# Kernel tuning notes

Measured on AMD Instinct MI355X. Metric: run time of the kernel, lower is better.

Reference implementation:

```python
import jax, jax.numpy as jnp
import numpy as np

EMBED_DIM = 1024
NUM_HEADS = 16
HEAD_DIM = EMBED_DIM // NUM_HEADS
QUANTUM_HEADS = 2
BATCH = 2
SEQ = 2048


def setup_inputs() -> dict:
    key = jax.random.key(0)
    ks = jax.random.split(key, 12)
    s = 1.0 / np.sqrt(EMBED_DIM)
    d = {
        "x": jax.random.normal(ks[0], (BATCH, SEQ, EMBED_DIM), jnp.float32),
        "Wq": jax.random.normal(ks[1], (EMBED_DIM, EMBED_DIM), jnp.float32) * s,
        "bq": jax.random.normal(ks[2], (EMBED_DIM,), jnp.float32) * s,
        "Wk": jax.random.normal(ks[3], (EMBED_DIM, EMBED_DIM), jnp.float32) * s,
        "bk": jax.random.normal(ks[4], (EMBED_DIM,), jnp.float32) * s,
        "Wv": jax.random.normal(ks[5], (EMBED_DIM, EMBED_DIM), jnp.float32) * s,
        "bv": jax.random.normal(ks[6], (EMBED_DIM,), jnp.float32) * s,
        "Wo": jax.random.normal(ks[7], (EMBED_DIM, EMBED_DIM), jnp.float32) * s,
        "bo": jax.random.normal(ks[8], (EMBED_DIM,), jnp.float32) * s,
        # surrogate params for the per-head quantum expectation layers
        "qw": jax.random.normal(ks[9], (QUANTUM_HEADS,), jnp.float32),
        "qb": jax.random.normal(ks[10], (QUANTUM_HEADS,), jnp.float32) * 0.1,
    }
    return d


def reference(x, Wq, bq, Wk, bk, Wv, bv, Wo, bo, qw, qb):
    B, S, E = x.shape
    H, D, QH = NUM_HEADS, HEAD_DIM, QUANTUM_HEADS

    def proj(W, b):  # nn.Linear: x @ W.T + b, then split heads -> (B,H,S,D)
        y = jnp.einsum("bse,fe->bsf", x, W) + b
        return y.reshape(B, S, H, D).transpose(0, 2, 1, 3)

    q = proj(Wq, bq)
    k = proj(Wk, bk)
    v = proj(Wv, bv)

    scores = jnp.einsum("bhsd,bhtd->bhst", q, k) / jnp.sqrt(jnp.float32(D))
    attn = jax.nn.softmax(scores, axis=-1)  # (B,H,S,S)

    # quantum-head post-softmax rescaling: per (batch, quantum head) scalar
    agg = attn[:, :QH].mean(axis=(2, 3))            # (B,QH)
    refined = jnp.cos(qw[None, :] * agg + qb[None, :])  # surrogate expectation in [-1,1]
    scale = jnp.concatenate(
        [refined, jnp.ones((B, H - QH), dtype=attn.dtype)], axis=1
    )  # (B,H)
    attn = attn * scale[:, :, None, None]

    out = jnp.einsum("bhst,bhtd->bhsd", attn, v)
    out = out.transpose(0, 2, 1, 3).reshape(B, S, E)
    out = jnp.einsum("bse,fe->bsf", out, Wo) + bo
    return out
```

## Files before the change

kernel.cpp:

```cpp
#include <hip/hip_runtime.h>
#include <hip/hip_bf16.h>

#define B_ 2
#define S_ 2048
#define E_ 1024
#define H_ 16
#define D_ 64

typedef __attribute__((ext_vector_type(8))) short short8;
typedef __attribute__((ext_vector_type(4))) float f32x4;
typedef __attribute__((ext_vector_type(4))) unsigned short u16x4;

#define AS1 __attribute__((address_space(1)))
#define AS3 __attribute__((address_space(3)))

static __device__ __forceinline__ unsigned short f2bf(float f) {
  unsigned int u = __builtin_bit_cast(unsigned int, f);
  unsigned int r = (u + 0x7fffu + ((u >> 16) & 1u)) >> 16;
  return (unsigned short)r;
}

static __device__ __forceinline__ void gload_lds16(const void* g, void* l) {
  __builtin_amdgcn_global_load_lds((const AS1 unsigned int*)g, (AS3 unsigned int*)l, 16, 0, 0);
}

__global__ __launch_bounds__(256) void cvt_bf16(const float* __restrict__ in,
                                                unsigned short* __restrict__ out, int n) {
  int i = (blockIdx.x * 256 + threadIdx.x) * 4;
  if (i >= n) return;
  f32x4 v = *(const f32x4*)(in + i);
  u16x4 o;
  o.x = f2bf(v.x); o.y = f2bf(v.y); o.z = f2bf(v.z); o.w = f2bf(v.w);
  *(u16x4*)(out + i) = o;
}

__global__ __launch_bounds__(256) void cvt_bf16_w4(const float* __restrict__ w0,
                                                   const float* __restrict__ w1,
                                                   const float* __restrict__ w2,
                                                   const float* __restrict__ w3,
                                                   unsigned short* __restrict__ out) {
  const float* src = (blockIdx.y == 0) ? w0 : (blockIdx.y == 1) ? w1 : (blockIdx.y == 2) ? w2 : w3;
  unsigned short* dst = out + (size_t)blockIdx.y * (E_ * E_);
  int i = (blockIdx.x * 256 + threadIdx.x) * 4;
  f32x4 v = *(const f32x4*)(src + i);
  u16x4 o;
  o.x = f2bf(v.x); o.y = f2bf(v.y); o.z = f2bf(v.z); o.w = f2bf(v.w);
  *(u16x4*)(dst + i) = o;
}

__global__ __launch_bounds__(256) void gemm_nt(const unsigned short* __restrict__ A,
                                               const unsigned short* __restrict__ W,
                                               const float* __restrict__ bias,
                                               void* __restrict__ Cout,
                                               int M, int N, int K, int out_bf16,
                                               float out_scale) {
  __shared__ unsigned short lA[64 * 32];
  __shared__ unsigned short lB[128 * 32];
  const int tid  = threadIdx.x;
  const int lane = tid & 63;
  const int w    = tid >> 6;
  const int m0   = blockIdx.x * 64;
  const int n0   = blockIdx.y * 128;
  const int mi   = (w >> 1) * 32;
  const int ni   = (w & 1) * 64;
  const int li   = lane & 15;
  const int quad = lane >> 4;
  const int koff = quad * 8;

  f32x4 acc[2][4];
#pragma unroll
  for (int i = 0; i < 2; ++i)
#pragma unroll
    for (int j = 0; j < 4; ++j) { f32x4 z = {0.f, 0.f, 0.f, 0.f}; acc[i][j] = z; }

  const int arow = tid >> 2, ak = (tid & 3) * 8;
  const int b2 = tid + 256;

  for (int k0 = 0; k0 < K; k0 += 32) {
    __syncthreads();
    gload_lds16(A + (size_t)(m0 + arow) * K + k0 + ak, &lA[tid * 8]);
    gload_lds16(W + (size_t)(n0 + arow) * K + k0 + ak, &lB[tid * 8]);
    gload_lds16(W + (size_t)(n0 + (b2 >> 2)) * K + k0 + (b2 & 3) * 8, &lB[b2 * 8]);
    __syncthreads();
    short8 a0 = *(const short8*)&lA[(mi      + li) * 32 + koff];
    short8 a1 = *(const short8*)&lA[(mi + 16 + li) * 32 + koff];
#pragma unroll
    for (int nt = 0; nt < 4; ++nt) {
      short8 bb = *(const short8*)&lB[(ni + nt * 16 + li) * 32 + koff];
      acc[0][nt] = __builtin_amdgcn_mfma_f32_16x16x32_bf16(a0, bb, acc[0][nt], 0, 0, 0);
      acc[1][nt] = __builtin_amdgcn_mfma_f32_16x16x32_bf16(a1, bb, acc[1][nt], 0, 0, 0);
    }
  }

#pragma unroll
  for (int mt = 0; mt < 2; ++mt)
#pragma unroll
    for (int nt = 0; nt < 4; ++nt) {
      int col = n0 + ni + nt * 16 + li;
      float bv = bias[col];
#pragma unroll
      for (int r = 0; r < 4; ++r) {
        int row = m0 + mi + mt * 16 + quad * 4 + r;
        float v = (acc[mt][nt][r] + bv) * out_scale;
        if (out_bf16) ((unsigned short*)Cout)[(size_t)row * N + col] = f2bf(v);
        else          ((float*)Cout)[(size_t)row * N + col] = v;
      }
    }
}

__global__ __launch_bounds__(256) void gemm_qkv(const unsigned short* __restrict__ A,
                                                const unsigned short* __restrict__ Wq,
                                                const unsigned short* __restrict__ Wk,
                                                const unsigned short* __restrict__ Wv,
                                                const float* __restrict__ bq,
                                                const float* __restrict__ bk,
                                                const float* __restrict__ bv,
                                                unsigned short* __restrict__ Qo,
                                                unsigned short* __restrict__ Ko,
                                                unsigned short* __restrict__ Vo) {
  const int z = blockIdx.z;
  const unsigned short* W = (z == 0) ? Wq : (z == 1) ? Wk : Wv;
  const float* bias = (z == 0) ? bq : (z == 1) ? bk : bv;
  unsigned short* C = (z == 0) ? Qo : (z == 1) ? Ko : Vo;
  const float out_scale = (z == 0) ? 0.125f : 1.0f;
  const int M = B_ * S_, N = E_, K = E_;

  __shared__ unsigned short lA[64 * 32];
  __shared__ unsigned short lB[128 * 32];
  const int tid  = threadIdx.x;
  const int lane = tid & 63;
  const int w    = tid >> 6;
  const int m0   = blockIdx.x * 64;
  const int n0   = blockIdx.y * 128;
  const int mi   = (w >> 1) * 32;
  const int ni   = (w & 1) * 64;
  const int li   = lane & 15;
  const int quad = lane >> 4;
  const int koff = quad * 8;

  f32x4 acc[2][4];
#pragma unroll
  for (int i = 0; i < 2; ++i)
#pragma unroll
    for (int j = 0; j < 4; ++j) { f32x4 z2 = {0.f, 0.f, 0.f, 0.f}; acc[i][j] = z2; }

  const int arow = tid >> 2, ak = (tid & 3) * 8;
  const int b2 = tid + 256;

  for (int k0 = 0; k0 < K; k0 += 32) {
    __syncthreads();
    gload_lds16(A + (size_t)(m0 + arow) * K + k0 + ak, &lA[tid * 8]);
    gload_lds16(W + (size_t)(n0 + arow) * K + k0 + ak, &lB[tid * 8]);
    gload_lds16(W + (size_t)(n0 + (b2 >> 2)) * K + k0 + (b2 & 3) * 8, &lB[b2 * 8]);
    __syncthreads();
    short8 a0 = *(const short8*)&lA[(mi      + li) * 32 + koff];
    short8 a1 = *(const short8*)&lA[(mi + 16 + li) * 32 + koff];
#pragma unroll
    for (int nt = 0; nt < 4; ++nt) {
      short8 bb = *(const short8*)&lB[(ni + nt * 16 + li) * 32 + koff];
      acc[0][nt] = __builtin_amdgcn_mfma_f32_16x16x32_bf16(a0, bb, acc[0][nt], 0, 0, 0);
      acc[1][nt] = __builtin_amdgcn_mfma_f32_16x16x32_bf16(a1, bb, acc[1][nt], 0, 0, 0);
    }
  }

#pragma unroll
  for (int mt = 0; mt < 2; ++mt)
#pragma unroll
    for (int nt = 0; nt < 4; ++nt) {
      int col = n0 + ni + nt * 16 + li;
      float bv = bias[col];
#pragma unroll
      for (int r = 0; r < 4; ++r) {
        int row = m0 + mi + mt * 16 + quad * 4 + r;
        C[(size_t)row * N + col] = f2bf((acc[mt][nt][r] + bv) * out_scale);
      }
    }
}

__global__ __launch_bounds__(256) void transpose_v(const unsigned short* __restrict__ V,
                                                   unsigned short* __restrict__ VT) {
  __shared__ unsigned short tile[64 * 72];
  const int tid = threadIdx.x;
  const int s0 = blockIdx.x * 64, h = blockIdx.y, b = blockIdx.z;
  {
    int rr = tid >> 2, c = (tid & 3) * 16;
    const unsigned short* src = V + ((size_t)(b * S_ + s0 + rr) * E_ + h * 64 + c);
    *(short8*)&tile[rr * 72 + c]     = *(const short8*)src;
    *(short8*)&tile[rr * 72 + c + 8] = *(const short8*)(src + 8);
  }
  __syncthreads();
  {
    int dr = tid >> 2, c = (tid & 3) * 16;
    short8 v0, v1;
#pragma unroll
    for (int u = 0; u < 8; ++u) v0[u] = (short)tile[(c + u) * 72 + dr];
#pragma unroll
    for (int u = 0; u < 8; ++u) v1[u] = (short)tile[(c + 8 + u) * 72 + dr];
    unsigned short* dst = VT + ((size_t)((b * H_ + h) * 64 + dr) * S_ + s0 + c);
    *(short8*)dst       = v0;
    *(short8*)(dst + 8) = v1;
  }
}

__global__ __launch_bounds__(256) void attn_kernel(const unsigned short* __restrict__ Q,
                                                   const unsigned short* __restrict__ Kp,
                                                   const unsigned short* __restrict__ VT,
                                                   const float* __restrict__ qw,
                                                   const float* __restrict__ qb,
                                                   unsigned short* __restrict__ O) {
  __shared__ unsigned short Qs[64 * 72];
  __shared__ unsigned short Ks[64 * 72];
  __shared__ unsigned short Vs[64 * 72];
  __shared__ unsigned short Ps[64 * 72];
  const int tid  = threadIdx.x;
  const int lane = tid & 63, w = tid >> 6;
  const int li   = lane & 15, quad = lane >> 4;
  const int s0 = blockIdx.x * 64, h = blockIdx.y, b = blockIdx.z;
  const int rr = tid >> 2, cc = (tid & 3) * 16;

  {
    const unsigned short* src = Q + ((size_t)(b * S_ + s0 + rr) * E_ + h * 64 + cc);
    *(short8*)&Qs[rr * 72 + cc]     = *(const short8*)src;
    *(short8*)&Qs[rr * 72 + cc + 8] = *(const short8*)(src + 8);
  }

  f32x4 oacc[4];
#pragma unroll
  for (int i = 0; i < 4; ++i) { f32x4 z = {0.f, 0.f, 0.f, 0.f}; oacc[i] = z; }
  float lacc[4] = {0.f, 0.f, 0.f, 0.f};

  for (int tt = 0; tt < S_ / 64; ++tt) {
    const int t0 = tt * 64;
    if (tt) __syncthreads();
    {
      const unsigned short* ksrc = Kp + ((size_t)(b * S_ + t0 + rr) * E_ + h * 64 + cc);
      *(short8*)&Ks[rr * 72 + cc]     = *(const short8*)ksrc;
      *(short8*)&Ks[rr * 72 + cc + 8] = *(const short8*)(ksrc + 8);
      const unsigned short* vsrc = VT + ((size_t)((b * H_ + h) * 64 + rr) * S_ + t0 + cc);
      *(short8*)&Vs[rr * 72 + cc]     = *(const short8*)vsrc;
      *(short8*)&Vs[rr * 72 + cc + 8] = *(const short8*)(vsrc + 8);
    }
    __syncthreads();

    f32x4 sacc[4];
#pragma unroll
    for (int i = 0; i < 4; ++i) { f32x4 z = {0.f, 0.f, 0.f, 0.f}; sacc[i] = z; }
#pragma unroll
    for (int ks = 0; ks < 2; ++ks) {
      short8 a = *(const short8*)&Qs[(w * 16 + li) * 72 + ks * 32 + quad * 8];
#pragma unroll
      for (int nt = 0; nt < 4; ++nt) {
        short8 bb = *(const short8*)&Ks[(nt * 16 + li) * 72 + ks * 32 + quad * 8];
        sacc[nt] = __builtin_amdgcn_mfma_f32_16x16x32_bf16(a, bb, sacc[nt], 0, 0, 0);
      }
    }

#pragma unroll
    for (int nt = 0; nt < 4; ++nt) {
#pragma unroll
      for (int r = 0; r < 4; ++r) {
        float p = __expf(sacc[nt][r]);
        lacc[r] += p;
        Ps[(w * 16 + quad * 4 + r) * 72 + nt * 16 + li] = f2bf(p);
      }
    }

#pragma unroll
    for (int ks = 0; ks < 2; ++ks) {
      short8 a = *(const short8*)&Ps[(w * 16 + li) * 72 + ks * 32 + quad * 8];
#pragma unroll
      for (int nt = 0; nt < 4; ++nt) {
        short8 bb = *(const short8*)&Vs[(nt * 16 + li) * 72 + ks * 32 + quad * 8];
        oacc[nt] = __builtin_amdgcn_mfma_f32_16x16x32_bf16(a, bb, oacc[nt], 0, 0, 0);
      }
    }
  }

  float lrow[4];
#pragma unroll
  for (int r = 0; r < 4; ++r) {
    float l = lacc[r];
    l += __shfl_xor(l, 1);
    l += __shfl_xor(l, 2);
    l += __shfl_xor(l, 4);
    l += __shfl_xor(l, 8);
    lrow[r] = l;
  }

  float scale = 1.0f;
  if (h < 2) scale = cosf(qw[h] * (1.0f / (float)S_) + qb[h]);
#pragma unroll
  for (int nt = 0; nt < 4; ++nt)
#pragma unroll
    for (int r = 0; r < 4; ++r) {
      float v = oacc[nt][r] / lrow[r] * scale;
      O[((size_t)(b * S_ + s0 + w * 16 + quad * 4 + r)) * E_ + h * 64 + nt * 16 + li] = f2bf(v);
    }
}

extern "C" void kernel_launch(void* const* d_in, const int* in_sizes, int n_in,
                              void* d_out, int out_size, void* d_ws, size_t ws_size,
                              hipStream_t stream) {
  const float* x  = (const float*)d_in[0];
  const float* Wq = (const float*)d_in[1];
  const float* bq = (const float*)d_in[2];
  const float* Wk = (const float*)d_in[3];
  const float* bk = (const float*)d_in[4];
  const float* Wv = (const float*)d_in[5];
  const float* bv = (const float*)d_in[6];
  const float* Wo = (const float*)d_in[7];
  const float* bo = (const float*)d_in[8];
  const float* qw = (const float*)d_in[9];
  const float* qb = (const float*)d_in[10];
  float* out = (float*)d_out;

  char* ws = (char*)d_ws;
  const size_t MB = 1u << 20;
  unsigned short* xb  = (unsigned short*)(ws + 0 * MB);
  unsigned short* Wqb = (unsigned short*)(ws + 8 * MB);
  unsigned short* Wkb = (unsigned short*)(ws + 10 * MB);
  unsigned short* Wvb = (unsigned short*)(ws + 12 * MB);
  unsigned short* Wob = (unsigned short*)(ws + 14 * MB);
  unsigned short* Qb  = (unsigned short*)(ws + 16 * MB);
  unsigned short* Kb  = (unsigned short*)(ws + 24 * MB);
  unsigned short* Vb  = (unsigned short*)(ws + 32 * MB);
  unsigned short* VTb = (unsigned short*)(ws + 40 * MB);
  unsigned short* Ob  = (unsigned short*)(ws + 48 * MB);

  cvt_bf16<<<4096, 256, 0, stream>>>(x, xb, B_ * S_ * E_);
  cvt_bf16_w4<<<dim3(1024, 4), 256, 0, stream>>>(Wq, Wk, Wv, Wo, Wqb);

  gemm_qkv<<<dim3(64, 8, 3), 256, 0, stream>>>(xb, Wqb, Wkb, Wvb, bq, bk, bv, Qb, Kb, Vb);

  transpose_v<<<dim3(S_ / 64, H_, B_), 256, 0, stream>>>(Vb, VTb);

  attn_kernel<<<dim3(S_ / 64, H_, B_), 256, 0, stream>>>(Qb, Kb, VTb, qw, qb, Ob);

  gemm_nt<<<dim3(64, 8), 256, 0, stream>>>(Ob, Wob, bo, (void*)out, B_ * S_, E_, E_, 0, 1.0f);
}
```

Before: 245.9 us.

## Enlarge GEMM tiles to 128x128, swizzle attention LDS, use 128-row attention blocks

Projection GEMMs move from 64x128 to 128x128 block tiles, so each wave computes 4x4 MFMA tiles, which raises reuse of each LDS fragment and halves the grid. The attention kernel now runs 512 threads over 128 query rows. It loads Q, K and V directly into LDS with global_load_lds, using an XOR-swizzled layout in place of padding to avoid bank conflicts, and it precomputes the LDS offsets. bf16 rounding switches to a cheaper round-half-up conversion, which slightly changes numerics. The larger tiles need more registers and leave fewer blocks to fill the CUs.

```diff
diff --git a/kernel.cpp b/kernel.cpp
--- a/kernel.cpp
+++ b/kernel.cpp
@@ -16,12 +16,17 @@
 
 static __device__ __forceinline__ unsigned short f2bf(float f) {
   unsigned int u = __builtin_bit_cast(unsigned int, f);
-  unsigned int r = (u + 0x7fffu + ((u >> 16) & 1u)) >> 16;
-  return (unsigned short)r;
-}
-
+  return (unsigned short)((u + 0x7fffu + ((u >> 16) & 1u)) >> 16);
+}
+static __device__ __forceinline__ unsigned short f2bf_f(float f) {
+  unsigned int u = __builtin_bit_cast(unsigned int, f);
+  return (unsigned short)((u + 0x8000u) >> 16);
+}
 static __device__ __forceinline__ void gload_lds16(const void* g, void* l) {
   __builtin_amdgcn_global_load_lds((const AS1 unsigned int*)g, (AS3 unsigned int*)l, 16, 0, 0);
+}
+static __device__ __forceinline__ int swz8(int row, int kc) {
+  return row * 64 + ((kc ^ (row & 7)) << 3);
 }
 
 __global__ __launch_bounds__(256) void cvt_bf16(const float* __restrict__ in,
@@ -48,64 +53,63 @@
   *(u16x4*)(dst + i) = o;
 }
 
-__global__ __launch_bounds__(256) void gemm_nt(const unsigned short* __restrict__ A,
-                                               const unsigned short* __restrict__ W,
-                                               const float* __restrict__ bias,
-                                               void* __restrict__ Cout,
-                                               int M, int N, int K, int out_bf16,
-                                               float out_scale) {
-  __shared__ unsigned short lA[64 * 32];
-  __shared__ unsigned short lB[128 * 32];
+static __device__ __forceinline__ void gemm128_body(
+    const unsigned short* __restrict__ A, const unsigned short* __restrict__ W,
+    const float* __restrict__ bias, void* __restrict__ Cout,
+    int N, int K, int out_bf16, float out_scale,
+    unsigned short* lA, unsigned short* lB) {
   const int tid  = threadIdx.x;
   const int lane = tid & 63;
   const int w    = tid >> 6;
-  const int m0   = blockIdx.x * 64;
-  const int n0   = blockIdx.y * 128;
-  const int mi   = (w >> 1) * 32;
-  const int ni   = (w & 1) * 64;
-  const int li   = lane & 15;
-  const int quad = lane >> 4;
-  const int koff = quad * 8;
-
-  f32x4 acc[2][4];
-#pragma unroll
-  for (int i = 0; i < 2; ++i)
+  const int wm   = (w >> 1) * 64, wn = (w & 1) * 64;
+  const int li   = lane & 15, quad = lane >> 4;
+  const int m0   = blockIdx.x * 128, n0 = blockIdx.y * 128;
+
+  f32x4 acc[4][4];
+#pragma unroll
+  for (int i = 0; i < 4; ++i)
 #pragma unroll
     for (int j = 0; j < 4; ++j) { f32x4 z = {0.f, 0.f, 0.f, 0.f}; acc[i][j] = z; }
 
-  const int arow = tid >> 2, ak = (tid & 3) * 8;
-  const int b2 = tid + 256;
+  const int r0 = tid >> 2, kc0 = (tid & 3) * 8;
+  const unsigned short* a0 = A + (size_t)(m0 + r0) * K + kc0;
+  const unsigned short* a1 = A + (size_t)(m0 + r0 + 64) * K + kc0;
+  const unsigned short* b0 = W + (size_t)(n0 + r0) * K + kc0;
+  const unsigned short* b1 = W + (size_t)(n0 + r0 + 64) * K + kc0;
 
   for (int k0 = 0; k0 < K; k0 += 32) {
     __syncthreads();
-    gload_lds16(A + (size_t)(m0 + arow) * K + k0 + ak, &lA[tid * 8]);
-    gload_lds16(W + (size_t)(n0 + arow) * K + k0 + ak, &lB[tid * 8]);
-    gload_lds16(W + (size_t)(n0 + (b2 >> 2)) * K + k0 + (b2 & 3) * 8, &lB[b2 * 8]);
+    gload_lds16(a0 + k0, &lA[tid * 8]);
+    gload_lds16(a1 + k0, &lA[(tid + 256) * 8]);
+    gload_lds16(b0 + k0, &lB[tid * 8]);
+    gload_lds16(b1 + k0, &lB[(tid + 256) * 8]);
     __syncthreads();
-    short8 a0 = *(const short8*)&lA[(mi      + li) * 32 + koff];
-    short8 a1 = *(const short8*)&lA[(mi + 16 + li) * 32 + koff];
-#pragma unroll
-    for (int nt = 0; nt < 4; ++nt) {
-      short8 bb = *(const short8*)&lB[(ni + nt * 16 + li) * 32 + koff];
-      acc[0][nt] = __builtin_amdgcn_mfma_f32_16x16x32_bf16(a0, bb, acc[0][nt], 0, 0, 0);
-      acc[1][nt] = __builtin_amdgcn_mfma_f32_16x16x32_bf16(a1, bb, acc[1][nt], 0, 0, 0);
-    }
-  }
-
-#pragma unroll
-  for (int mt = 0; mt < 2; ++mt)
-#pragma unroll
-    for (int nt = 0; nt < 4; ++nt) {
-      int col = n0 + ni + nt * 16 + li;
-      float bv = bias[col];
+    short8 af[4], bf[4];
+#pragma unroll
+    for (int i = 0; i < 4; ++i) af[i] = *(const short8*)&lA[(wm + i * 16 + li) * 32 + quad * 8];
+#pragma unroll
+    for (int j = 0; j < 4; ++j) bf[j] = *(const short8*)&lB[(wn + j * 16 + li) * 32 + quad * 8];
+#pragma unroll
+    for (int i = 0; i < 4; ++i)
+#pragma unroll
+      for (int j = 0; j < 4; ++j)
+        acc[i][j] = __builtin_amdgcn_mfma_f32_16x16x32_bf16(af[i], bf[j], acc[i][j], 0, 0, 0);
+  }
+
+#pragma unroll
+  for (int j = 0; j < 4; ++j) {
+    int col = n0 + wn + j * 16 + li;
+    float bv = bias[col];
+#pragma unroll
+    for (int i = 0; i < 4; ++i)
 #pragma unroll
       for (int r = 0; r < 4; ++r) {
-        int row = m0 + mi + mt * 16 + quad * 4 + r;
-        float v = (acc[mt][nt][r] + bv) * out_scale;
-        if (out_bf16) ((unsigned short*)Cout)[(size_t)row * N + col] = f2bf(v);
+        int row = m0 + wm + i * 16 + quad * 4 + r;
+        float v = (acc[i][j][r] + bv) * out_scale;
+        if (out_bf16) ((unsigned short*)Cout)[(size_t)row * N + col] = f2bf_f(v);
         else          ((float*)Cout)[(size_t)row * N + col] = v;
       }
-    }
+  }
 }
 
 __global__ __launch_bounds__(256) void gemm_qkv(const unsigned short* __restrict__ A,
@@ -118,63 +122,23 @@
                                                 unsigned short* __restrict__ Qo,
                                                 unsigned short* __restrict__ Ko,
                                                 unsigned short* __restrict__ Vo) {
+  __shared__ unsigned short lA[128 * 32];
+  __shared__ unsigned short lB[128 * 32];
   const int z = blockIdx.z;
   const unsigned short* W = (z == 0) ? Wq : (z == 1) ? Wk : Wv;
   const float* bias = (z == 0) ? bq : (z == 1) ? bk : bv;
   unsigned short* C = (z == 0) ? Qo : (z == 1) ? Ko : Vo;
-  const float out_scale = (z == 0) ? 0.125f : 1.0f;
-  const int M = B_ * S_, N = E_, K = E_;
-
-  __shared__ unsigned short lA[64 * 32];
+  const float sc = (z == 0) ? 0.125f : 1.0f;
+  gemm128_body(A, W, bias, (void*)C, E_, E_, 1, sc, lA, lB);
+}
+
+__global__ __launch_bounds__(256) void gemm_out(const unsigned short* __restrict__ A,
+                                                const unsigned short* __restrict__ W,
+                                                const float* __restrict__ bias,
+                                                float* __restrict__ C) {
+  __shared__ unsigned short lA[128 * 32];
   __shared__ unsigned short lB[128 * 32];
-  const int tid  = threadIdx.x;
-  const int lane = tid & 63;
-  const int w    = tid >> 6;
-  const int m0   = blockIdx.x * 64;
-  const int n0   = blockIdx.y * 128;
-  const int mi   = (w >> 1) * 32;
-  const int ni   = (w & 1) * 64;
-  const int li   = lane & 15;
-  const int quad = lane >> 4;
-  const int koff = quad * 8;
-
-  f32x4 acc[2][4];
-#pragma unroll
-  for (int i = 0; i < 2; ++i)
-#pragma unroll
-    for (int j = 0; j < 4; ++j) { f32x4 z2 = {0.f, 0.f, 0.f, 0.f}; acc[i][j] = z2; }
-
-  const int arow = tid >> 2, ak = (tid & 3) * 8;
-  const int b2 = tid + 256;
-
-  for (int k0 = 0; k0 < K; k0 += 32) {
-    __syncthreads();
-    gload_lds16(A + (size_t)(m0 + arow) * K + k0 + ak, &lA[tid * 8]);
-    gload_lds16(W + (size_t)(n0 + arow) * K + k0 + ak, &lB[tid * 8]);
-    gload_lds16(W + (size_t)(n0 + (b2 >> 2)) * K + k0 + (b2 & 3) * 8, &lB[b2 * 8]);
-    __syncthreads();
-    short8 a0 = *(const short8*)&lA[(mi      + li) * 32 + koff];
-    short8 a1 = *(const short8*)&lA[(mi + 16 + li) * 32 + koff];
-#pragma unroll
-    for (int nt = 0; nt < 4; ++nt) {
-      short8 bb = *(const short8*)&lB[(ni + nt * 16 + li) * 32 + koff];
-      acc[0][nt] = __builtin_amdgcn_mfma_f32_16x16x32_bf16(a0, bb, acc[0][nt], 0, 0, 0);
-      acc[1][nt] = __builtin_amdgcn_mfma_f32_16x16x32_bf16(a1, bb, acc[1][nt], 0, 0, 0);
-    }
-  }
-
-#pragma unroll
-  for (int mt = 0; mt < 2; ++mt)
-#pragma unroll
-    for (int nt = 0; nt < 4; ++nt) {
-      int col = n0 + ni + nt * 16 + li;
-      float bv = bias[col];
-#pragma unroll
-      for (int r = 0; r < 4; ++r) {
-        int row = m0 + mi + mt * 16 + quad * 4 + r;
-        C[(size_t)row * N + col] = f2bf((acc[mt][nt][r] + bv) * out_scale);
-      }
-    }
+  gemm128_body(A, W, bias, (void*)C, E_, E_, 0, 1.0f, lA, lB);
 }
 
 __global__ __launch_bounds__(256) void transpose_v(const unsigned short* __restrict__ V,
@@ -202,77 +166,89 @@
   }
 }
 
-__global__ __launch_bounds__(256) void attn_kernel(const unsigned short* __restrict__ Q,
+__global__ __launch_bounds__(512) void attn_kernel(const unsigned short* __restrict__ Q,
                                                    const unsigned short* __restrict__ Kp,
                                                    const unsigned short* __restrict__ VT,
                                                    const float* __restrict__ qw,
                                                    const float* __restrict__ qb,
                                                    unsigned short* __restrict__ O) {
-  __shared__ unsigned short Qs[64 * 72];
-  __shared__ unsigned short Ks[64 * 72];
-  __shared__ unsigned short Vs[64 * 72];
-  __shared__ unsigned short Ps[64 * 72];
+  __shared__ unsigned short Qs[128 * 64];
+  __shared__ unsigned short Ks[64 * 64];
+  __shared__ unsigned short Vs[64 * 64];
+  __shared__ unsigned short Ps[128 * 64];
   const int tid  = threadIdx.x;
   const int lane = tid & 63, w = tid >> 6;
   const int li   = lane & 15, quad = lane >> 4;
-  const int s0 = blockIdx.x * 64, h = blockIdx.y, b = blockIdx.z;
-  const int rr = tid >> 2, cc = (tid & 3) * 16;
+  const int s0 = blockIdx.x * 128, h = blockIdx.y, b = blockIdx.z;
 
   {
-    const unsigned short* src = Q + ((size_t)(b * S_ + s0 + rr) * E_ + h * 64 + cc);
-    *(short8*)&Qs[rr * 72 + cc]     = *(const short8*)src;
-    *(short8*)&Qs[rr * 72 + cc + 8] = *(const short8*)(src + 8);
-  }
+    int c = tid, r = c >> 3, kcl = (c & 7) ^ (r & 7);
+    gload_lds16(Q + (size_t)(b * S_ + s0 + r) * E_ + h * 64 + kcl * 8, &Qs[c * 8]);
+    c = tid + 512; r = c >> 3; kcl = (c & 7) ^ (r & 7);
+    gload_lds16(Q + (size_t)(b * S_ + s0 + r) * E_ + h * 64 + kcl * 8, &Qs[c * 8]);
+  }
+  const int srow = tid >> 3, skc = (tid & 7) ^ (srow & 7);
+  const unsigned short* kptr = Kp + (size_t)(b * S_ + srow) * E_ + h * 64 + skc * 8;
+  const unsigned short* vptr = VT + ((size_t)((b * H_ + h) * 64 + srow)) * S_ + skc * 8;
 
   f32x4 oacc[4];
 #pragma unroll
   for (int i = 0; i < 4; ++i) { f32x4 z = {0.f, 0.f, 0.f, 0.f}; oacc[i] = z; }
   float lacc[4] = {0.f, 0.f, 0.f, 0.f};
 
+  const int arow = w * 16 + li;
+  const int aoff0 = swz8(arow, quad);
+  const int aoff1 = swz8(arow, 4 + quad);
+  int boff[2][4];
+#pragma unroll
+  for (int ks = 0; ks < 2; ++ks)
+#pragma unroll
+    for (int nt = 0; nt < 4; ++nt) boff[ks][nt] = swz8(nt * 16 + li, ks * 4 + quad);
+  int pwo[4][4];
+#pragma unroll
+  for (int nt = 0; nt < 4; ++nt)
+#pragma unroll
+    for (int r = 0; r < 4; ++r)
+      pwo[nt][r] = swz8(w * 16 + quad * 4 + r, 2 * nt + (li >> 3)) + (li & 7);
+
   for (int tt = 0; tt < S_ / 64; ++tt) {
-    const int t0 = tt * 64;
-    if (tt) __syncthreads();
-    {
-      const unsigned short* ksrc = Kp + ((size_t)(b * S_ + t0 + rr) * E_ + h * 64 + cc);
-      *(short8*)&Ks[rr * 72 + cc]     = *(const short8*)ksrc;
-      *(short8*)&Ks[rr * 72 + cc + 8] = *(const short8*)(ksrc + 8);
-      const unsigned short* vsrc = VT + ((size_t)((b * H_ + h) * 64 + rr) * S_ + t0 + cc);
-      *(short8*)&Vs[rr * 72 + cc]     = *(const short8*)vsrc;
-      *(short8*)&Vs[rr * 72 + cc + 8] = *(const short8*)(vsrc + 8);
+    __syncthreads();
+    gload_lds16(kptr, &Ks[tid * 8]);
+    gload_lds16(vptr, &Vs[tid * 8]);
+    kptr += (size_t)64 * E_;
+    vptr += 64;
+    __syncthreads();
+
+    f32x4 sacc[4];
+#pragma unroll
+    for (int i = 0; i < 4; ++i) { f32x4 z = {0.f, 0.f, 0.f, 0.f}; sacc[i] = z; }
+    short8 qa0 = *(const short8*)&Qs[aoff0];
+    short8 qa1 = *(const short8*)&Qs[aoff1];
+#pragma unroll
+    for (int nt = 0; nt < 4; ++nt) {
+      short8 k0 = *(const short8*)&Ks[boff[0][nt]];
+      short8 k1 = *(const short8*)&Ks[boff[1][nt]];
+      sacc[nt] = __builtin_amdgcn_mfma_f32_16x16x32_bf16(qa0, k0, sacc[nt], 0, 0, 0);
+      sacc[nt] = __builtin_amdgcn_mfma_f32_16x16x32_bf16(qa1, k1, sacc[nt], 0, 0, 0);
     }
-    __syncthreads();
-
-    f32x4 sacc[4];
-#pragma unroll
-    for (int i = 0; i < 4; ++i) { f32x4 z = {0.f, 0.f, 0.f, 0.f}; sacc[i] = z; }
-#pragma unroll
-    for (int ks = 0; ks < 2; ++ks) {
-      short8 a = *(const short8*)&Qs[(w * 16 + li) * 72 + ks * 32 + quad * 8];
-#pragma unroll
-      for (int nt = 0; nt < 4; ++nt) {
-        short8 bb = *(const short8*)&Ks[(nt * 16 + li) * 72 + ks * 32 + quad * 8];
-        sacc[nt] = __builtin_amdgcn_mfma_f32_16x16x32_bf16(a, bb, sacc[nt], 0, 0, 0);
-      }
-    }
-
-#pragma unroll
-    for (int nt = 0; nt < 4; ++nt) {
+
+#pragma unroll
+    for (int nt = 0; nt < 4; ++nt)
 #pragma unroll
       for (int r = 0; r < 4; ++r) {
         float p = __expf(sacc[nt][r]);
         lacc[r] += p;
-        Ps[(w * 16 + quad * 4 + r) * 72 + nt * 16 + li] = f2bf(p);
+        Ps[pwo[nt][r]] = f2bf_f(p);
       }
-    }
-
-#pragma unroll
-    for (int ks = 0; ks < 2; ++ks) {
-      short8 a = *(const short8*)&Ps[(w * 16 + li) * 72 + ks * 32 + quad * 8];
-#pragma unroll
-      for (int nt = 0; nt < 4; ++nt) {
-        short8 bb = *(const short8*)&Vs[(nt * 16 + li) * 72 + ks * 32 + quad * 8];
-        oacc[nt] = __builtin_amdgcn_mfma_f32_16x16x32_bf16(a, bb, oacc[nt], 0, 0, 0);
-      }
+
+    short8 pa0 = *(const short8*)&Ps[aoff0];
+    short8 pa1 = *(const short8*)&Ps[aoff1];
+#pragma unroll
+    for (int nt = 0; nt < 4; ++nt) {
+      short8 v0 = *(const short8*)&Vs[boff[0][nt]];
+      short8 v1 = *(const short8*)&Vs[boff[1][nt]];
+      oacc[nt] = __builtin_amdgcn_mfma_f32_16x16x32_bf16(pa0, v0, oacc[nt], 0, 0, 0);
+      oacc[nt] = __builtin_amdgcn_mfma_f32_16x16x32_bf16(pa1, v1, oacc[nt], 0, 0, 0);
     }
   }
 
@@ -294,7 +270,7 @@
 #pragma unroll
     for (int r = 0; r < 4; ++r) {
       float v = oacc[nt][r] / lrow[r] * scale;
-      O[((size_t)(b * S_ + s0 + w * 16 + quad * 4 + r)) * E_ + h * 64 + nt * 16 + li] = f2bf(v);
+      O[((size_t)(b * S_ + s0 + w * 16 + quad * 4 + r)) * E_ + h * 64 + nt * 16 + li] = f2bf_f(v);
     }
 }
 
@@ -330,11 +306,11 @@
   cvt_bf16<<<4096, 256, 0, stream>>>(x, xb, B_ * S_ * E_);
   cvt_bf16_w4<<<dim3(1024, 4), 256, 0, stream>>>(Wq, Wk, Wv, Wo, Wqb);
 
-  gemm_qkv<<<dim3(64, 8, 3), 256, 0, stream>>>(xb, Wqb, Wkb, Wvb, bq, bk, bv, Qb, Kb, Vb);
+  gemm_qkv<<<dim3(32, 8, 3), 256, 0, stream>>>(xb, Wqb, Wkb, Wvb, bq, bk, bv, Qb, Kb, Vb);
 
   transpose_v<<<dim3(S_ / 64, H_, B_), 256, 0, stream>>>(Vb, VTb);
 
-  attn_kernel<<<dim3(S_ / 64, H_, B_), 256, 0, stream>>>(Qb, Kb, VTb, qw, qb, Ob);
-
-  gemm_nt<<<dim3(64, 8), 256, 0, stream>>>(Ob, Wob, bo, (void*)out, B_ * S_, E_, E_, 0, 1.0f);
-}
+  attn_kernel<<<dim3(S_ / 128, H_, B_), 512, 0, stream>>>(Qb, Kb, VTb, qw, qb, Ob);
+
+  gemm_out<<<dim3(32, 8), 256, 0, stream>>>(Ob, Wob, bo, out);
+}
```

New measurement: 211.6 us. 1.16x faster.
